# Optimization experiments

Hardware: AMD Instinct MI355X
Metric: run time of the kernel (lower is better)

The kernel has to match this reference:

```python
import jax, jax.numpy as jnp
import numpy as np

EPS = 1e-09


def _glorot(key, shape):
    fan_in, fan_out = shape[-2], shape[-1]
    std = (2.0 / (fan_in + fan_out)) ** 0.5
    return jax.random.normal(key, shape, dtype=jnp.float32) * std


def setup_inputs() -> dict:
    key = jax.random.key(0)
    kx, k1, k2, k3, k4 = jax.random.split(key, 5)
    B, S, D = 2, 1024, 256
    H, K = 8, 32  # key_dim_frac = 1/8
    return {
        "x": jax.random.normal(kx, (B, S, D), dtype=jnp.float32),
        "Wks": _glorot(k1, (H, D, K)),
        "Wqs": _glorot(k2, (H, D, K)),
        "Wvs": _glorot(k3, (H, D, D)),
        "Wo": _glorot(k4, (H, D, D)),
    }


def reference(x, Wks, Wqs, Wvs, Wo):
    # Per-head projections: [H, B, S, K] / [H, B, S, D]
    keys = jnp.einsum('bsd,hdk->hbsk', x, Wks)
    queries = jnp.einsum('bsd,hdk->hbsk', x, Wqs)
    values = jnp.einsum('bsd,hde->hbse', x, Wvs)

    # Feature map: elu + 1 (strictly positive)
    keys = jax.nn.elu(keys) + 1.0
    queries = jax.nn.elu(queries) + 1.0

    # Auxiliary pairwise attention map [H, B, S, S], causal-masked, row-normalized
    att = jnp.einsum('hbsk,hbtk->hbst', queries, keys)
    S = att.shape[-1]
    causal = jnp.tril(jnp.ones((S, S), dtype=att.dtype))
    att = att * causal
    att = att / (jnp.sum(att, axis=-1, keepdims=True) + EPS)

    # Causal linear attention via cumulative sums of outer products
    # [H, B, S, D, K] cumulative state (memory-bound, mirrors tf.cumsum)
    kv = jnp.einsum('hbsk,hbsd->hbsdk', keys, values)
    kv_cum = jnp.cumsum(kv, axis=2)
    numerator = jnp.einsum('hbsdk,hbsk->hbsd', kv_cum, queries)
    denominator = jnp.einsum('hbsk,hbsk->hbs', jnp.cumsum(keys, axis=2), queries)
    node = numerator / (denominator[..., None] + EPS)

    # Output projection, summed over heads: [B, S, D]
    out = jnp.einsum('hbsd,hde->bse', node, Wo)
    return (out, att)
```

## Files before the change

kernel.cpp:

```cpp
#include <hip/hip_runtime.h>
#include <hip/hip_bf16.h>
#include <cstdio>

#define PB 2
#define PS 1024
#define PD 256
#define PK 32
#define PH 8
#define HB (PH*PB)
#define BS (PB*PS)
#define EPS 1e-9f

typedef __attribute__((ext_vector_type(8))) short bf16x8;
typedef __attribute__((ext_vector_type(4))) float f32x4;

__device__ inline unsigned short f2bf(float f) {
    __hip_bfloat16 h = __float2bfloat16(f);
    return *reinterpret_cast<unsigned short*>(&h);
}
__device__ inline float bf2f(unsigned short u) {
    return __bfloat162float(*reinterpret_cast<__hip_bfloat16*>(&u));
}

__global__ __launch_bounds__(256) void k_prep(
    const float* __restrict__ x, const float* __restrict__ Wqs,
    const float* __restrict__ Wks, const float* __restrict__ Wvs,
    const float* __restrict__ Wo,
    unsigned short* __restrict__ xb, unsigned short* __restrict__ WqT,
    unsigned short* __restrict__ WkT, unsigned short* __restrict__ WvT,
    unsigned short* __restrict__ WoT)
{
    __shared__ float smem[8448];
    int bid = blockIdx.x, tid = threadIdx.x;
    if (bid < 512) {
        int i = bid*256 + tid;
        float4 v = ((const float4*)x)[i];
        ushort4 o = {f2bf(v.x), f2bf(v.y), f2bf(v.z), f2bf(v.w)};
        ((ushort4*)xb)[i] = o;
        return;
    }
    if (bid < 528) {
        int r2 = bid - 512;
        int h = r2 >> 1, isK = r2 & 1;
        const float* S = (isK ? Wks : Wqs) + (size_t)h*8192;
        unsigned short* D = (isK ? WkT : WqT) + (size_t)h*8192;
#pragma unroll
        for (int p = 0; p < 32; ++p) {
            int idx = p*256 + tid;
            smem[(idx>>5)*33 + (idx&31)] = S[idx];
        }
        __syncthreads();
#pragma unroll
        for (int p = 0; p < 8; ++p) {
            int o4 = p*256 + tid;
            int kk = o4 >> 6, d = (o4 & 63)*4;
            ushort4 o;
            o.x = f2bf(smem[(d+0)*33 + kk]); o.y = f2bf(smem[(d+1)*33 + kk]);
            o.z = f2bf(smem[(d+2)*33 + kk]); o.w = f2bf(smem[(d+3)*33 + kk]);
            *(ushort4*)(D + (size_t)kk*256 + d) = o;
        }
        return;
    }
    int r3 = bid - 528;
    const float* S; unsigned short* dst; int rs, hs;
    if (r3 < 128) { S = Wvs; dst = WvT; rs = 256;  hs = 65536; }
    else          { r3 -= 128; S = Wo; dst = WoT; rs = 2048; hs = 256; }
    int e0 = (r3 & 3)*64, d0 = ((r3>>2) & 3)*64, h = r3 >> 4;
    float (*T)[69] = (float(*)[69])smem;
    const float* Sh = S + (size_t)h*65536;
    int ty = tid>>4, c4 = tid&15;
#pragma unroll
    for (int p = 0; p < 4; ++p) {
        int r = p*16 + ty;
        float4 v = *(const float4*)(Sh + (size_t)(d0+r)*256 + e0 + c4*4);
        T[r][c4*4+0]=v.x; T[r][c4*4+1]=v.y; T[r][c4*4+2]=v.z; T[r][c4*4+3]=v.w;
    }
    __syncthreads();
    unsigned short* D = dst + (size_t)h*hs;
#pragma unroll
    for (int p = 0; p < 4; ++p) {
        int er = p*16 + ty;
        ushort4 o;
        o.x = f2bf(T[c4*4+0][er]); o.y = f2bf(T[c4*4+1][er]);
        o.z = f2bf(T[c4*4+2][er]); o.w = f2bf(T[c4*4+3][er]);
        *(ushort4*)(D + (size_t)(e0+er)*rs + d0 + c4*4) = o;
    }
}

__global__ __launch_bounds__(256) void k_proj(
    const unsigned short* __restrict__ xb, const unsigned short* __restrict__ WqT,
    const unsigned short* __restrict__ WkT, const unsigned short* __restrict__ WvT,
    unsigned short* __restrict__ Qb, unsigned short* __restrict__ Kb,
    unsigned short* __restrict__ Vt)
{
    int z = blockIdx.z;
    int m0 = blockIdx.y*64, n0 = blockIdx.x*64;
    int tid = threadIdx.x, w = tid>>6, l15 = tid&15, g = (tid>>4)&3;
    f32x4 zf = {0.f,0.f,0.f,0.f};
    f32x4 acc[4] = {zf,zf,zf,zf};
    const unsigned short* arow = xb + (size_t)(m0+16*w+l15)*256 + 8*g;
    const unsigned short* W;
    if (z < 8)       W = WvT + (size_t)z*65536;
    else if (z == 8) W = WqT;
    else             W = WkT;
#pragma unroll
    for (int kk = 0; kk < 8; ++kk) {
        bf16x8 af = *(const bf16x8*)(arow + kk*32);
#pragma unroll
        for (int nt = 0; nt < 4; ++nt) {
            bf16x8 bf = *(const bf16x8*)(W + (size_t)(n0+16*nt+l15)*256 + kk*32 + 8*g);
            acc[nt] = __builtin_amdgcn_mfma_f32_16x16x32_bf16(af, bf, acc[nt], 0, 0, 0);
        }
    }
    if (z < 8) {
        unsigned short* VtT = Vt + ((size_t)z*32 + blockIdx.y)*(256*64);
#pragma unroll
        for (int nt = 0; nt < 4; ++nt) {
            ushort4 o = {f2bf(acc[nt][0]), f2bf(acc[nt][1]), f2bf(acc[nt][2]), f2bf(acc[nt][3])};
            *(ushort4*)(VtT + (size_t)(n0+16*nt+l15)*64 + 16*w + 4*g) = o;
        }
    } else {
        unsigned short* dst = (z == 8) ? Qb : Kb;
        int bs_base = m0 + 16*w + 4*g;
#pragma unroll
        for (int nt = 0; nt < 4; ++nt) {
            int col = n0 + 16*nt + l15;
            int h = col>>5, kk = col&31;
#pragma unroll
            for (int j = 0; j < 4; ++j) {
                int bs = bs_base + j;
                int b = bs>>10, s = bs&1023;
                float zv = acc[nt][j];
                zv = zv > 0.f ? zv + 1.f : expf(zv);
                dst[((size_t)(h*PB+b)*PS + s)*PK + kk] = f2bf(zv);
            }
        }
    }
}

__global__ __launch_bounds__(256) void k_kv_sums(
    const unsigned short* __restrict__ Kb, const unsigned short* __restrict__ Vt,
    float* __restrict__ KVs, float* __restrict__ Ksum)
{
    int c = blockIdx.x, hb = blockIdx.y;
    int tid = threadIdx.x, w = tid>>6, l15 = tid&15, g = (tid>>4)&3;
    __shared__ unsigned short KT[32*72];
    __shared__ float partial[8][32];
#pragma unroll
    for (int i = 0; i < 8; ++i) {
        int flat = tid + i*256;
        KT[(flat&31)*72 + (flat>>5)] = Kb[((size_t)hb*PS + c*64 + (flat>>5))*PK + (flat&31)];
    }
    __syncthreads();
    {
        int kk = tid & 31, part = tid >> 5;
        float s = 0.f;
#pragma unroll
        for (int i = 0; i < 8; ++i) s += bf2f(KT[kk*72 + part*8 + i]);
        partial[part][kk] = s;
    }
    const unsigned short* Vtt = Vt + ((size_t)hb*16 + c)*(256*64);
    f32x4 zf = {0.f,0.f,0.f,0.f};
    f32x4 acc[4][2];
#pragma unroll
    for (int mt = 0; mt < 4; ++mt) { acc[mt][0] = zf; acc[mt][1] = zf; }
#pragma unroll
    for (int ks = 0; ks < 2; ++ks) {
        bf16x8 af[4];
#pragma unroll
        for (int mt = 0; mt < 4; ++mt)
            af[mt] = *(const bf16x8*)(Vtt + (size_t)(64*w + 16*mt + l15)*64 + 32*ks + 8*g);
#pragma unroll
        for (int nt = 0; nt < 2; ++nt) {
            bf16x8 bf = *(const bf16x8*)(KT + (16*nt + l15)*72 + 32*ks + 8*g);
#pragma unroll
            for (int mt = 0; mt < 4; ++mt)
                acc[mt][nt] = __builtin_amdgcn_mfma_f32_16x16x32_bf16(af[mt], bf, acc[mt][nt], 0, 0, 0);
        }
    }
    __syncthreads();
    if (tid < 32) {
        float s = 0.f;
#pragma unroll
        for (int p = 0; p < 8; ++p) s += partial[p][tid];
        Ksum[((size_t)hb*16 + c)*32 + tid] = s;
    }
    float* o = KVs + ((size_t)hb*16 + c)*8192;
#pragma unroll
    for (int mt = 0; mt < 4; ++mt)
#pragma unroll
        for (int nt = 0; nt < 2; ++nt)
#pragma unroll
            for (int j = 0; j < 4; ++j)
                o[(size_t)(64*w + 16*mt + 4*g + j)*32 + 16*nt + l15] = acc[mt][nt][j];
}

__global__ __launch_bounds__(256) void k_mid(
    const float* __restrict__ KVs, const float* __restrict__ Ksum,
    const unsigned short* __restrict__ Qb, const unsigned short* __restrict__ Kb,
    unsigned short* __restrict__ KVpre, float* __restrict__ den)
{
    int hb = blockIdx.y;
    int xb_ = blockIdx.x;
    __shared__ float kc[64][33];
    if (xb_ < 32) {
        int i = xb_*256 + threadIdx.x;
        const float* src = KVs + (size_t)hb*16*8192 + i;
        unsigned short* dst = KVpre + (size_t)hb*16*8192 + i;
        float acc = 0.f;
#pragma unroll
        for (int cc = 0; cc < 16; ++cc) { dst[cc*8192] = f2bf(acc); acc += src[cc*8192]; }
        return;
    }
    int c = xb_ - 32;
    int tid = threadIdx.x;
    int r = tid >> 2, quad = tid & 3;
    bf16x8 k8 = *(const bf16x8*)(Kb + ((size_t)hb*PS + c*64 + r)*PK + quad*8);
#pragma unroll
    for (int i = 0; i < 8; ++i) kc[r][quad*8+i] = bf2f((unsigned short)k8[i]);
    __syncthreads();
#pragma unroll
    for (int st = 1; st < 64; st <<= 1) {
        float tmp[8];
#pragma unroll
        for (int i = 0; i < 8; ++i) tmp[i] = (r >= st) ? kc[r-st][quad*8+i] : 0.f;
        __syncthreads();
#pragma unroll
        for (int i = 0; i < 8; ++i) kc[r][quad*8+i] += tmp[i];
        __syncthreads();
    }
    float kp[8];
#pragma unroll
    for (int i = 0; i < 8; ++i) kp[i] = 0.f;
    for (int cc = 0; cc < c; ++cc) {
        const float* Ks = Ksum + ((size_t)hb*16 + cc)*32 + quad*8;
#pragma unroll
        for (int i = 0; i < 8; ++i) kp[i] += Ks[i];
    }
    bf16x8 q8 = *(const bf16x8*)(Qb + ((size_t)hb*PS + c*64 + r)*PK + quad*8);
    float p = 0.f;
#pragma unroll
    for (int i = 0; i < 8; ++i)
        p += bf2f((unsigned short)q8[i]) * (kp[i] + kc[r][quad*8+i]);
    p += __shfl_xor(p, 1);
    p += __shfl_xor(p, 2);
    if (quad == 0) den[hb*PS + c*64 + r] = p + EPS;
}

__global__ __launch_bounds__(256) void k_att_panel(
    const unsigned short* __restrict__ Qb, const unsigned short* __restrict__ Kb,
    const float* __restrict__ den, float* __restrict__ att)
{
    int panel = blockIdx.x, hb = blockIdx.y;
    int s0 = panel*16;
    int tid = threadIdx.x, w = tid>>6, l15 = tid&15, g = (tid>>4)&3;
    __shared__ float P[16*1024];
    f32x4 zf = {0.f,0.f,0.f,0.f};

    float rd[4];
#pragma unroll
    for (int j = 0; j < 4; ++j) rd[j] = 1.0f / den[hb*PS + s0 + 4*g + j];

    bf16x8 qf = *(const bf16x8*)(Qb + ((size_t)hb*PS + s0 + l15)*PK + 8*g);

#pragma unroll
    for (int i = 0; i < 16; ++i) {
        int ct = i*4 + w;
        int t0 = ct*16;
        int col = t0 + l15;
        if (t0 > s0 + 15) {
#pragma unroll
            for (int j = 0; j < 4; ++j) P[(4*g + j)*1024 + col] = 0.f;
            continue;
        }
        bf16x8 kf = *(const bf16x8*)(Kb + ((size_t)hb*PS + col)*PK + 8*g);
        f32x4 p = __builtin_amdgcn_mfma_f32_16x16x32_bf16(qf, kf, zf, 0, 0, 0);
#pragma unroll
        for (int j = 0; j < 4; ++j) {
            int r = 4*g + j;
            float v = p[j] * rd[j];
            if (col > s0 + r) v = 0.f;
            P[r*1024 + col] = v;
        }
    }
    __syncthreads();
    float* dst = att + (size_t)hb*PS*PS + (size_t)s0*PS;
#pragma unroll
    for (int i = 0; i < 16; ++i) {
        f32x4 v = *(const f32x4*)&P[i*1024 + tid*4];
        __builtin_nontemporal_store(v, (f32x4*)(dst + (size_t)i*PS + tid*4));
    }
}

__global__ __launch_bounds__(256) void k_node(
    const unsigned short* __restrict__ Qb, const unsigned short* __restrict__ Kb,
    const float* __restrict__ den, const unsigned short* __restrict__ Vt,
    const unsigned short* __restrict__ KVpre,
    unsigned short* __restrict__ nodeB)
{
    int c = blockIdx.x, hb = blockIdx.y;
    int s0 = c*64;
    int tid = threadIdx.x, w = tid>>6, l15 = tid&15, g = (tid>>4)&3;
    __shared__ unsigned short PL[64*72];
    __shared__ float rden[64];
    if (tid < 64) rden[tid] = 1.0f / den[hb*PS + s0 + tid];

    f32x4 zf = {0.f,0.f,0.f,0.f};
    bf16x8 qf = *(const bf16x8*)(Qb + ((size_t)hb*PS + s0 + 16*w + l15)*PK + 8*g);

    const unsigned short* KVp = KVpre + ((size_t)hb*16 + c)*8192;
    f32x4 acc[16];
#pragma unroll
    for (int nt = 0; nt < 16; ++nt) {
        bf16x8 bf = *(const bf16x8*)(KVp + (size_t)(16*nt + l15)*32 + 8*g);
        acc[nt] = __builtin_amdgcn_mfma_f32_16x16x32_bf16(qf, bf, zf, 0, 0, 0);
    }
    f32x4 p[4];
#pragma unroll
    for (int nt4 = 0; nt4 < 4; ++nt4) {
        bf16x8 kf = *(const bf16x8*)(Kb + ((size_t)hb*PS + s0 + 16*nt4 + l15)*PK + 8*g);
        p[nt4] = __builtin_amdgcn_mfma_f32_16x16x32_bf16(qf, kf, zf, 0, 0, 0);
    }
    __syncthreads();
#pragma unroll
    for (int nt4 = 0; nt4 < 4; ++nt4) {
#pragma unroll
        for (int j = 0; j < 4; ++j) {
            int r = 16*w + 4*g + j;
            int tc = 16*nt4 + l15;
            float v = p[nt4][j] * rden[r];
            if (tc > r) v = 0.f;
            PL[r*72 + tc] = f2bf(v);
        }
    }
#pragma unroll
    for (int nt = 0; nt < 16; ++nt)
#pragma unroll
        for (int j = 0; j < 4; ++j)
            acc[nt][j] *= rden[16*w + 4*g + j];
    __syncthreads();
    const unsigned short* Vtt = Vt + ((size_t)hb*16 + c)*(256*64);
#pragma unroll
    for (int ks = 0; ks < 2; ++ks) {
        bf16x8 af = *(const bf16x8*)(PL + (size_t)(16*w + l15)*72 + 32*ks + 8*g);
#pragma unroll
        for (int nt = 0; nt < 16; ++nt) {
            bf16x8 vf = *(const bf16x8*)(Vtt + (size_t)(16*nt + l15)*64 + 32*ks + 8*g);
            acc[nt] = __builtin_amdgcn_mfma_f32_16x16x32_bf16(af, vf, acc[nt], 0, 0, 0);
        }
    }
    int h = hb >> 1, b = hb & 1;
    unsigned short* np = nodeB + ((size_t)(b*PS + s0))*2048 + h*256;
#pragma unroll
    for (int nt = 0; nt < 16; ++nt)
#pragma unroll
        for (int j = 0; j < 4; ++j)
            np[(size_t)(16*w + 4*g + j)*2048 + 16*nt + l15] = f2bf(acc[nt][j]);
}

__global__ __launch_bounds__(256) void k_out2(
    const unsigned short* __restrict__ nodeB, const unsigned short* __restrict__ WoT,
    float* __restrict__ out)
{
    int e0 = blockIdx.x*64, m0 = blockIdx.y*16;
    int tid = threadIdx.x, w = tid>>6, l15 = tid&15, g = (tid>>4)&3;
    f32x4 zf = {0.f,0.f,0.f,0.f};
    f32x4 acc = zf;
    const unsigned short* arow = nodeB + (size_t)(m0 + l15)*2048 + 8*g;
    const unsigned short* brow = WoT + (size_t)(e0 + 16*w + l15)*2048 + 8*g;
#pragma unroll 8
    for (int kk = 0; kk < 64; ++kk) {
        bf16x8 af = *(const bf16x8*)(arow + kk*32);
        bf16x8 bf = *(const bf16x8*)(brow + kk*32);
        acc = __builtin_amdgcn_mfma_f32_16x16x32_bf16(af, bf, acc, 0, 0, 0);
    }
#pragma unroll
    for (int j = 0; j < 4; ++j)
        __builtin_nontemporal_store(acc[j], out + (size_t)(m0 + 4*g + j)*PD + e0 + 16*w + l15);
}

extern "C" void kernel_launch(void* const* d_in, const int* in_sizes, int n_in,
                              void* d_out, int out_size, void* d_ws, size_t ws_size,
                              hipStream_t stream) {
    const float* x   = (const float*)d_in[0];
    const float* Wks = (const float*)d_in[1];
    const float* Wqs = (const float*)d_in[2];
    const float* Wvs = (const float*)d_in[3];
    const float* Wo  = (const float*)d_in[4];

    float* out = (float*)d_out;
    float* att = (float*)d_out + (size_t)PB*PS*PD;

    float* ws = (float*)d_ws;
    float*          den   = ws + 0;
    unsigned short* Qb    = (unsigned short*)(ws + 16384);
    unsigned short* Kb    = (unsigned short*)(ws + 278528);
    unsigned short* Vt    = (unsigned short*)(ws + 540672);
    unsigned short* xb    = (unsigned short*)(ws + 2637824);
    unsigned short* WqT   = (unsigned short*)(ws + 2899968);
    unsigned short* WkT   = (unsigned short*)(ws + 2932736);
    unsigned short* WvT   = (unsigned short*)(ws + 2965504);
    unsigned short* WoT   = (unsigned short*)(ws + 3227648);
    unsigned short* nodeB = (unsigned short*)(ws + 3489792);
    float*          KVs   = ws + 5586944;
    unsigned short* KVpre = (unsigned short*)(ws + 7684096);
    float*          KsumG = ws + 8732672;
    const size_t needed = (size_t)8740864 * 4;
    if (ws_size < needed) {
        fprintf(stderr, "kernel_launch: ws_size %zu < needed %zu\n", ws_size, needed);
        return;
    }

    k_prep<<<784, 256, 0, stream>>>(x, Wqs, Wks, Wvs, Wo, xb, WqT, WkT, WvT, WoT);
    k_proj<<<dim3(4, 32, 10), 256, 0, stream>>>(xb, WqT, WkT, WvT, Qb, Kb, Vt);
    k_kv_sums<<<dim3(16, HB), 256, 0, stream>>>(Kb, Vt, KVs, KsumG);
    k_mid<<<dim3(48, HB), 256, 0, stream>>>(KVs, KsumG, Qb, Kb, KVpre, den);
    k_att_panel<<<dim3(64, HB), 256, 0, stream>>>(Qb, Kb, den, att);
    k_node<<<dim3(16, HB), 256, 0, stream>>>(Qb, Kb, den, Vt, KVpre, nodeB);
    k_out2<<<dim3(4, 128), 256, 0, stream>>>(nodeB, WoT, out);
}
```

Baseline: 105.1 us.

## Fuse x bf16 conversion into projection GEMM and coalesce stores via LDS staging

Drops the separate x-to-bf16 pass from k_prep. k_proj now loads fp32 x directly, converts it into shared memory, and stages its Q/K/V outputs through LDS so they go out as coalesced 16-byte stores instead of scattered 2-byte writes. k_node also stages its output tile through LDS for vectorized stores. k_att_panel is split into four column quarters per panel, which cuts shared memory per block and quadruples the grid for better occupancy. The cost is that each of the ten z-slices of k_proj re-reads and re-converts x, plus more shared memory and extra barriers.

```diff
diff --git a/kernel.cpp b/kernel.cpp
--- a/kernel.cpp
+++ b/kernel.cpp
@@ -23,25 +23,15 @@
 }
 
 __global__ __launch_bounds__(256) void k_prep(
-    const float* __restrict__ x, const float* __restrict__ Wqs,
-    const float* __restrict__ Wks, const float* __restrict__ Wvs,
-    const float* __restrict__ Wo,
-    unsigned short* __restrict__ xb, unsigned short* __restrict__ WqT,
-    unsigned short* __restrict__ WkT, unsigned short* __restrict__ WvT,
-    unsigned short* __restrict__ WoT)
+    const float* __restrict__ Wqs, const float* __restrict__ Wks,
+    const float* __restrict__ Wvs, const float* __restrict__ Wo,
+    unsigned short* __restrict__ WqT, unsigned short* __restrict__ WkT,
+    unsigned short* __restrict__ WvT, unsigned short* __restrict__ WoT)
 {
     __shared__ float smem[8448];
     int bid = blockIdx.x, tid = threadIdx.x;
-    if (bid < 512) {
-        int i = bid*256 + tid;
-        float4 v = ((const float4*)x)[i];
-        ushort4 o = {f2bf(v.x), f2bf(v.y), f2bf(v.z), f2bf(v.w)};
-        ((ushort4*)xb)[i] = o;
-        return;
-    }
-    if (bid < 528) {
-        int r2 = bid - 512;
-        int h = r2 >> 1, isK = r2 & 1;
+    if (bid < 16) {
+        int h = bid >> 1, isK = bid & 1;
         const float* S = (isK ? Wks : Wqs) + (size_t)h*8192;
         unsigned short* D = (isK ? WkT : WqT) + (size_t)h*8192;
 #pragma unroll
@@ -61,7 +51,7 @@
         }
         return;
     }
-    int r3 = bid - 528;
+    int r3 = bid - 16;
     const float* S; unsigned short* dst; int rs, hs;
     if (r3 < 128) { S = Wvs; dst = WvT; rs = 256;  hs = 65536; }
     else          { r3 -= 128; S = Wo; dst = WoT; rs = 2048; hs = 256; }
@@ -88,7 +78,7 @@
 }
 
 __global__ __launch_bounds__(256) void k_proj(
-    const unsigned short* __restrict__ xb, const unsigned short* __restrict__ WqT,
+    const float* __restrict__ xg, const unsigned short* __restrict__ WqT,
     const unsigned short* __restrict__ WkT, const unsigned short* __restrict__ WvT,
     unsigned short* __restrict__ Qb, unsigned short* __restrict__ Kb,
     unsigned short* __restrict__ Vt)
@@ -96,16 +86,28 @@
     int z = blockIdx.z;
     int m0 = blockIdx.y*64, n0 = blockIdx.x*64;
     int tid = threadIdx.x, w = tid>>6, l15 = tid&15, g = (tid>>4)&3;
-    f32x4 zf = {0.f,0.f,0.f,0.f};
-    f32x4 acc[4] = {zf,zf,zf,zf};
-    const unsigned short* arow = xb + (size_t)(m0+16*w+l15)*256 + 8*g;
+    __shared__ unsigned short xs[64][280];
+    __shared__ unsigned short os[64][72];
+
+#pragma unroll
+    for (int p = 0; p < 16; ++p) {
+        int idx = tid + p*256;
+        int row = idx >> 6, c4 = idx & 63;
+        float4 v = *(const float4*)(xg + (size_t)(m0+row)*256 + c4*4);
+        ushort4 o = {f2bf(v.x), f2bf(v.y), f2bf(v.z), f2bf(v.w)};
+        *(ushort4*)&xs[row][c4*4] = o;
+    }
     const unsigned short* W;
     if (z < 8)       W = WvT + (size_t)z*65536;
     else if (z == 8) W = WqT;
     else             W = WkT;
+    __syncthreads();
+
+    f32x4 zf = {0.f,0.f,0.f,0.f};
+    f32x4 acc[4] = {zf,zf,zf,zf};
 #pragma unroll
     for (int kk = 0; kk < 8; ++kk) {
-        bf16x8 af = *(const bf16x8*)(arow + kk*32);
+        bf16x8 af = *(const bf16x8*)&xs[16*w + l15][kk*32 + 8*g];
 #pragma unroll
         for (int nt = 0; nt < 4; ++nt) {
             bf16x8 bf = *(const bf16x8*)(W + (size_t)(n0+16*nt+l15)*256 + kk*32 + 8*g);
@@ -113,27 +115,38 @@
         }
     }
     if (z < 8) {
-        unsigned short* VtT = Vt + ((size_t)z*32 + blockIdx.y)*(256*64);
-#pragma unroll
-        for (int nt = 0; nt < 4; ++nt) {
-            ushort4 o = {f2bf(acc[nt][0]), f2bf(acc[nt][1]), f2bf(acc[nt][2]), f2bf(acc[nt][3])};
-            *(ushort4*)(VtT + (size_t)(n0+16*nt+l15)*64 + 16*w + 4*g) = o;
+#pragma unroll
+        for (int nt = 0; nt < 4; ++nt)
+#pragma unroll
+            for (int j = 0; j < 4; ++j)
+                os[16*nt + l15][16*w + 4*g + j] = f2bf(acc[nt][j]);
+        __syncthreads();
+        float4* dstb = (float4*)(Vt + ((size_t)z*32 + blockIdx.y)*16384 + (size_t)n0*64);
+#pragma unroll
+        for (int p = 0; p < 2; ++p) {
+            int idx = tid + p*256;
+            int e = idx >> 3, c8 = idx & 7;
+            dstb[idx] = *(const float4*)&os[e][c8*8];
         }
     } else {
         unsigned short* dst = (z == 8) ? Qb : Kb;
-        int bs_base = m0 + 16*w + 4*g;
-#pragma unroll
-        for (int nt = 0; nt < 4; ++nt) {
-            int col = n0 + 16*nt + l15;
-            int h = col>>5, kk = col&31;
+#pragma unroll
+        for (int nt = 0; nt < 4; ++nt)
 #pragma unroll
             for (int j = 0; j < 4; ++j) {
-                int bs = bs_base + j;
-                int b = bs>>10, s = bs&1023;
                 float zv = acc[nt][j];
                 zv = zv > 0.f ? zv + 1.f : expf(zv);
-                dst[((size_t)(h*PB+b)*PS + s)*PK + kk] = f2bf(zv);
+                os[16*w + 4*g + j][16*nt + l15] = f2bf(zv);
             }
+        __syncthreads();
+        int b = m0 >> 10, s0 = m0 & 1023, h0 = n0 >> 5;
+#pragma unroll
+        for (int p = 0; p < 2; ++p) {
+            int idx = tid + p*256;
+            int hh = idx >> 8, fi = idx & 255;
+            int s = fi >> 2, kk8 = fi & 3;
+            float4* base = (float4*)(dst + ((size_t)((h0+hh)*PB + b)*PS + s0)*PK);
+            base[fi] = *(const float4*)&os[s][hh*32 + kk8*8];
         }
     }
 }
@@ -251,10 +264,11 @@
     const unsigned short* __restrict__ Qb, const unsigned short* __restrict__ Kb,
     const float* __restrict__ den, float* __restrict__ att)
 {
-    int panel = blockIdx.x, hb = blockIdx.y;
-    int s0 = panel*16;
+    int pid = blockIdx.x, hb = blockIdx.y;
+    int panel = pid >> 2, cq = pid & 3;
+    int s0 = panel*16, c0 = cq*256;
     int tid = threadIdx.x, w = tid>>6, l15 = tid&15, g = (tid>>4)&3;
-    __shared__ float P[16*1024];
+    __shared__ float P[16][260];
     f32x4 zf = {0.f,0.f,0.f,0.f};
 
     float rd[4];
@@ -264,13 +278,13 @@
     bf16x8 qf = *(const bf16x8*)(Qb + ((size_t)hb*PS + s0 + l15)*PK + 8*g);
 
 #pragma unroll
-    for (int i = 0; i < 16; ++i) {
+    for (int i = 0; i < 4; ++i) {
         int ct = i*4 + w;
-        int t0 = ct*16;
+        int t0 = c0 + ct*16;
         int col = t0 + l15;
         if (t0 > s0 + 15) {
 #pragma unroll
-            for (int j = 0; j < 4; ++j) P[(4*g + j)*1024 + col] = 0.f;
+            for (int j = 0; j < 4; ++j) P[4*g + j][t0 - c0 + l15] = 0.f;
             continue;
         }
         bf16x8 kf = *(const bf16x8*)(Kb + ((size_t)hb*PS + col)*PK + 8*g);
@@ -280,15 +294,17 @@
             int r = 4*g + j;
             float v = p[j] * rd[j];
             if (col > s0 + r) v = 0.f;
-            P[r*1024 + col] = v;
-        }
-    }
-    __syncthreads();
-    float* dst = att + (size_t)hb*PS*PS + (size_t)s0*PS;
-#pragma unroll
-    for (int i = 0; i < 16; ++i) {
-        f32x4 v = *(const f32x4*)&P[i*1024 + tid*4];
-        __builtin_nontemporal_store(v, (f32x4*)(dst + (size_t)i*PS + tid*4));
+            P[r][col - c0] = v;
+        }
+    }
+    __syncthreads();
+    float* dst = att + (size_t)hb*PS*PS + (size_t)s0*PS + c0;
+#pragma unroll
+    for (int p = 0; p < 4; ++p) {
+        int idx = tid + p*256;
+        int r = idx >> 6, c = idx & 63;
+        f32x4 v = *(const f32x4*)&P[r][c*4];
+        __builtin_nontemporal_store(v, (f32x4*)(dst + (size_t)r*PS + c*4));
     }
 }
 
@@ -302,6 +318,7 @@
     int s0 = c*64;
     int tid = threadIdx.x, w = tid>>6, l15 = tid&15, g = (tid>>4)&3;
     __shared__ unsigned short PL[64*72];
+    __shared__ unsigned short ns[64][272];
     __shared__ float rden[64];
     if (tid < 64) rden[tid] = 1.0f / den[hb*PS + s0 + tid];
 
@@ -349,13 +366,20 @@
             acc[nt] = __builtin_amdgcn_mfma_f32_16x16x32_bf16(af, vf, acc[nt], 0, 0, 0);
         }
     }
+#pragma unroll
+    for (int nt = 0; nt < 16; ++nt)
+#pragma unroll
+        for (int j = 0; j < 4; ++j)
+            ns[16*w + 4*g + j][16*nt + l15] = f2bf(acc[nt][j]);
+    __syncthreads();
     int h = hb >> 1, b = hb & 1;
-    unsigned short* np = nodeB + ((size_t)(b*PS + s0))*2048 + h*256;
-#pragma unroll
-    for (int nt = 0; nt < 16; ++nt)
-#pragma unroll
-        for (int j = 0; j < 4; ++j)
-            np[(size_t)(16*w + 4*g + j)*2048 + 16*nt + l15] = f2bf(acc[nt][j]);
+#pragma unroll
+    for (int p2 = 0; p2 < 8; ++p2) {
+        int idx = tid + p2*256;
+        int row = idx >> 5, c8 = idx & 31;
+        float4* dstp = (float4*)(nodeB + ((size_t)(b*PS + s0 + row))*2048 + h*256);
+        dstp[c8] = *(const float4*)&ns[row][c8*8];
+    }
 }
 
 __global__ __launch_bounds__(256) void k_out2(
@@ -396,7 +420,6 @@
     unsigned short* Qb    = (unsigned short*)(ws + 16384);
     unsigned short* Kb    = (unsigned short*)(ws + 278528);
     unsigned short* Vt    = (unsigned short*)(ws + 540672);
-    unsigned short* xb    = (unsigned short*)(ws + 2637824);
     unsigned short* WqT   = (unsigned short*)(ws + 2899968);
     unsigned short* WkT   = (unsigned short*)(ws + 2932736);
     unsigned short* WvT   = (unsigned short*)(ws + 2965504);
@@ -411,11 +434,11 @@
         return;
     }
 
-    k_prep<<<784, 256, 0, stream>>>(x, Wqs, Wks, Wvs, Wo, xb, WqT, WkT, WvT, WoT);
-    k_proj<<<dim3(4, 32, 10), 256, 0, stream>>>(xb, WqT, WkT, WvT, Qb, Kb, Vt);
+    k_prep<<<272, 256, 0, stream>>>(Wqs, Wks, Wvs, Wo, WqT, WkT, WvT, WoT);
+    k_proj<<<dim3(4, 32, 10), 256, 0, stream>>>(x, WqT, WkT, WvT, Qb, Kb, Vt);
     k_kv_sums<<<dim3(16, HB), 256, 0, stream>>>(Kb, Vt, KVs, KsumG);
     k_mid<<<dim3(48, HB), 256, 0, stream>>>(KVs, KsumG, Qb, Kb, KVpre, den);
-    k_att_panel<<<dim3(64, HB), 256, 0, stream>>>(Qb, Kb, den, att);
+    k_att_panel<<<dim3(256, HB), 256, 0, stream>>>(Qb, Kb, den, att);
     k_node<<<dim3(16, HB), 256, 0, stream>>>(Qb, Kb, den, Vt, KVpre, nodeB);
     k_out2<<<dim3(4, 128), 256, 0, stream>>>(nodeB, WoT, out);
 }
```

Result: no change. 103.8 us (-1.2%).

## Split attention panels into column quarters and stage node output through LDS

Applied to the files above, without the earlier changes.

The attention-map kernel now splits each 16-row panel into four 256-column chunks. That gives four times as many blocks, each with a smaller LDS buffer padded to cut bank conflicts, which should raise occupancy on the bandwidth-bound 64MB att write. Separately, k_node writes its bf16 results to a padded shared tile and then stores to nodeB with coalesced 16-byte writes instead of scattered 2-byte stores. The cost is an extra barrier and more LDS in k_node, plus repeated Q and denominator loads across the column quarters.

```diff
diff --git a/kernel.cpp b/kernel.cpp
--- a/kernel.cpp
+++ b/kernel.cpp
@@ -251,10 +251,11 @@
     const unsigned short* __restrict__ Qb, const unsigned short* __restrict__ Kb,
     const float* __restrict__ den, float* __restrict__ att)
 {
-    int panel = blockIdx.x, hb = blockIdx.y;
-    int s0 = panel*16;
+    int pid = blockIdx.x, hb = blockIdx.y;
+    int panel = pid >> 2, cq = pid & 3;
+    int s0 = panel*16, c0 = cq*256;
     int tid = threadIdx.x, w = tid>>6, l15 = tid&15, g = (tid>>4)&3;
-    __shared__ float P[16*1024];
+    __shared__ float P[16][260];
     f32x4 zf = {0.f,0.f,0.f,0.f};
 
     float rd[4];
@@ -264,13 +265,13 @@
     bf16x8 qf = *(const bf16x8*)(Qb + ((size_t)hb*PS + s0 + l15)*PK + 8*g);
 
 #pragma unroll
-    for (int i = 0; i < 16; ++i) {
+    for (int i = 0; i < 4; ++i) {
         int ct = i*4 + w;
-        int t0 = ct*16;
+        int t0 = c0 + ct*16;
         int col = t0 + l15;
         if (t0 > s0 + 15) {
 #pragma unroll
-            for (int j = 0; j < 4; ++j) P[(4*g + j)*1024 + col] = 0.f;
+            for (int j = 0; j < 4; ++j) P[4*g + j][t0 - c0 + l15] = 0.f;
             continue;
         }
         bf16x8 kf = *(const bf16x8*)(Kb + ((size_t)hb*PS + col)*PK + 8*g);
@@ -280,15 +281,17 @@
             int r = 4*g + j;
             float v = p[j] * rd[j];
             if (col > s0 + r) v = 0.f;
-            P[r*1024 + col] = v;
-        }
-    }
-    __syncthreads();
-    float* dst = att + (size_t)hb*PS*PS + (size_t)s0*PS;
-#pragma unroll
-    for (int i = 0; i < 16; ++i) {
-        f32x4 v = *(const f32x4*)&P[i*1024 + tid*4];
-        __builtin_nontemporal_store(v, (f32x4*)(dst + (size_t)i*PS + tid*4));
+            P[r][col - c0] = v;
+        }
+    }
+    __syncthreads();
+    float* dst = att + (size_t)hb*PS*PS + (size_t)s0*PS + c0;
+#pragma unroll
+    for (int p = 0; p < 4; ++p) {
+        int idx = tid + p*256;
+        int r = idx >> 6, c = idx & 63;
+        f32x4 v = *(const f32x4*)&P[r][c*4];
+        __builtin_nontemporal_store(v, (f32x4*)(dst + (size_t)r*PS + c*4));
     }
 }
 
@@ -302,6 +305,7 @@
     int s0 = c*64;
     int tid = threadIdx.x, w = tid>>6, l15 = tid&15, g = (tid>>4)&3;
     __shared__ unsigned short PL[64*72];
+    __shared__ unsigned short ns[64][272];
     __shared__ float rden[64];
     if (tid < 64) rden[tid] = 1.0f / den[hb*PS + s0 + tid];
 
@@ -349,13 +353,20 @@
             acc[nt] = __builtin_amdgcn_mfma_f32_16x16x32_bf16(af, vf, acc[nt], 0, 0, 0);
         }
     }
+#pragma unroll
+    for (int nt = 0; nt < 16; ++nt)
+#pragma unroll
+        for (int j = 0; j < 4; ++j)
+            ns[16*w + 4*g + j][16*nt + l15] = f2bf(acc[nt][j]);
+    __syncthreads();
     int h = hb >> 1, b = hb & 1;
-    unsigned short* np = nodeB + ((size_t)(b*PS + s0))*2048 + h*256;
-#pragma unroll
-    for (int nt = 0; nt < 16; ++nt)
-#pragma unroll
-        for (int j = 0; j < 4; ++j)
-            np[(size_t)(16*w + 4*g + j)*2048 + 16*nt + l15] = f2bf(acc[nt][j]);
+#pragma unroll
+    for (int p2 = 0; p2 < 8; ++p2) {
+        int idx = tid + p2*256;
+        int row = idx >> 5, c8 = idx & 31;
+        float4* dstp = (float4*)(nodeB + ((size_t)(b*PS + s0 + row))*2048 + h*256);
+        dstp[c8] = *(const float4*)&ns[row][c8*8];
+    }
 }
 
 __global__ __launch_bounds__(256) void k_out2(
@@ -415,7 +426,7 @@
     k_proj<<<dim3(4, 32, 10), 256, 0, stream>>>(xb, WqT, WkT, WvT, Qb, Kb, Vt);
     k_kv_sums<<<dim3(16, HB), 256, 0, stream>>>(Kb, Vt, KVs, KsumG);
     k_mid<<<dim3(48, HB), 256, 0, stream>>>(KVs, KsumG, Qb, Kb, KVpre, den);
-    k_att_panel<<<dim3(64, HB), 256, 0, stream>>>(Qb, Kb, den, att);
+    k_att_panel<<<dim3(256, HB), 256, 0, stream>>>(Qb, Kb, den, att);
     k_node<<<dim3(16, HB), 256, 0, stream>>>(Qb, Kb, den, Vt, KVpre, nodeB);
     k_out2<<<dim3(4, 128), 256, 0, stream>>>(nodeB, WoT, out);
 }
```

Result: no change. 106.1 us (+0.9%).
